# Kernel tuning notes

Measured on AMD Instinct MI355X. Metric: run time of the kernel, lower is better.

The kernel has to match this reference:

```python
import jax, jax.numpy as jnp
import numpy as np


def setup_inputs() -> dict:
    key = jax.random.key(0)
    k1, k2, k3, k4 = jax.random.split(key, 4)
    batch, T, state_dim, action_dim = 64, 1024, 512, 128
    x0 = jax.random.normal(k1, (batch, state_dim), dtype=jnp.float32)
    us = jax.random.normal(k2, (batch, T, action_dim), dtype=jnp.float32)
    # Scale A so the 1024-step linear recurrence stays bounded (spectral radius < 1)
    A = jax.random.normal(k3, (state_dim, state_dim), dtype=jnp.float32) * (0.9 / np.sqrt(state_dim))
    B = jax.random.normal(k4, (action_dim, state_dim), dtype=jnp.float32) * (1.0 / np.sqrt(action_dim))
    return {"x0": x0, "us": us, "A": A, "B": B}


def reference(x0, us, A, B):
    """Linear SSM rollout: x_{t+1} = x_t @ A + u_t @ B, returns xs [batch, T, state_dim]."""
    us_t = jnp.swapaxes(us, 0, 1)  # [T, batch, action_dim]

    def step(x, u):
        x_next = x @ A + u @ B  # [batch, state_dim]
        return x_next, x_next

    _, xs = jax.lax.scan(step, x0, us_t)  # xs: [T, batch, state_dim]
    return jnp.swapaxes(xs, 0, 1)  # [batch, T, state_dim]
```

## Files before the change

### kernel.cpp

```cpp
#include <hip/hip_runtime.h>


typedef __attribute__((ext_vector_type(8))) short bf16x8;
typedef __attribute__((ext_vector_type(8))) unsigned short ushort8;
typedef __attribute__((ext_vector_type(4))) float f32x4;
typedef unsigned short ushort_t;

#define MFMA16(a, b, c) __builtin_amdgcn_mfma_f32_16x16x32_bf16(a, b, c, 0, 0, 0)

#define OFF_AT  0UL
#define OFF_AU  8912896UL
#define OFF_BT  15204352UL
#define OFF_BU  15335424UL
#define OFF_WT  15466496UL
#define OFF_Z   16515072UL
#define OFF_E1S 41680896UL
#define OFF_E2S 50069504UL

__host__ __device__ __forceinline__ int slot_of(int p) {
    if (p == 0) return 16;
    if (p <= 8) return p - 1;
    return 7 + (p >> 3);
}

__device__ __forceinline__ unsigned short f2bf(float f) {
    union { float f; unsigned u; } v; v.f = f;
    unsigned r = v.u + 0x7FFFu + ((v.u >> 16) & 1u);
    return (unsigned short)(r >> 16);
}

__device__ __forceinline__ int sel4(int4 v, int p) {
    return p == 0 ? v.x : p == 1 ? v.y : p == 2 ? v.z : v.w;
}

typedef __attribute__((address_space(3))) unsigned int as3_u32;
typedef __attribute__((address_space(1))) const unsigned int as1_u32;
__device__ __forceinline__ void gll16(const void* g, void* l) {
    __builtin_amdgcn_global_load_lds((as1_u32*)g, (as3_u32*)l, 16, 0, 0);
}

__global__ __launch_bounds__(256) void prep_kernel(const float* __restrict__ x0,
                                                   const float* __restrict__ us,
                                                   const float* __restrict__ A,
                                                   const float* __restrict__ B,
                                                   char* __restrict__ ws) {
    ushort_t* At1 = (ushort_t*)(ws + OFF_AT);
    ushort_t* Au1 = (ushort_t*)(ws + OFF_AU);
    ushort_t* Bt  = (ushort_t*)(ws + OFF_BT);
    ushort_t* Bu  = (ushort_t*)(ws + OFF_BU);
    ushort_t* X0b = (ushort_t*)(ws + OFF_E2S);
    ushort_t* Z   = (ushort_t*)(ws + OFF_Z);
    long idx = (long)blockIdx.x * 256 + threadIdx.x;
    if (idx < 262144) {
        Au1[idx] = f2bf(A[idx]);
    } else if (idx < 524288) {
        long gi = idx - 262144;
        int n = (int)(gi >> 9), k = (int)(gi & 511);
        At1[gi] = f2bf(A[(long)k * 512 + n]);
    } else if (idx < 589824) {
        long i2 = idx - 524288;
        int kp = (int)(i2 >> 9), n = (int)(i2 & 511);
        ushort_t v = f2bf(B[i2]);
        Bt[(long)n * 128 + kp] = v;
        Bu[i2] = v;
    } else if (idx < 593920) {
        long gi = idx - 589824;
        long e0 = gi * 8;
        float4 v0 = *(const float4*)(x0 + e0);
        float4 v1 = *(const float4*)(x0 + e0 + 4);
        ushort8 h = { f2bf(v0.x), f2bf(v0.y), f2bf(v0.z), f2bf(v0.w),
                      f2bf(v1.x), f2bf(v1.y), f2bf(v1.z), f2bf(v1.w) };
        *(ushort8*)(X0b + e0) = h;
    } else if (idx < 1642496) {
        long gi = idx - 593920;
        int row = (int)(gi >> 7), g8 = (int)(gi & 127);
        int c = row >> 6, b = row & 63;
        const float* src = us + (long)b * 131072 + c * 1024 + g8 * 8;
        float4 v0 = *(const float4*)src;
        float4 v1 = *(const float4*)(src + 4);
        ushort8 h = { f2bf(v0.x), f2bf(v0.y), f2bf(v0.z), f2bf(v0.w),
                      f2bf(v1.x), f2bf(v1.y), f2bf(v1.z), f2bf(v1.w) };
        *(ushort8*)(Z + (long)row * 1536 + 512 + g8 * 8) = h;
    } else {
        long gi2 = idx - 1642496;
        if (gi2 < 262144) {
            int n = (int)(gi2 >> 9), k2 = (int)(gi2 & 511);
            At1[(long)16 * 262144 + gi2] = (n == k2) ? (ushort_t)0x3F80 : (ushort_t)0;
        }
    }
}

__device__ __forceinline__ void pow_tile(char* __restrict__ ws, ushort_t* ldsX,
                                         int d, int m_, int i_, int prod,
                                         int mb, int nb) {
    ushort_t* At = (ushort_t*)(ws + OFF_AT);
    ushort_t* Au = (ushort_t*)(ws + OFF_AU);
    const ushort_t *Xp, *Yp; ushort_t* outp;
    if (prod == 0) { Xp = At + (long)slot_of(m_) * 262144; Yp = Au + (long)slot_of(i_) * 262144; outp = At + (long)slot_of(d) * 262144; }
    else           { Xp = Au + (long)slot_of(i_) * 262144; Yp = At + (long)slot_of(m_) * 262144; outp = Au + (long)slot_of(d) * 262144; }

    int tid = threadIdx.x, w = tid >> 6, lane = tid & 63, q = lane >> 4, r = lane & 15;

    for (int i2 = tid; i2 < 64 * 64; i2 += 256) {
        int row = i2 >> 6, c8 = i2 & 63;
        ushort8 v = *(const ushort8*)(Xp + (long)(mb * 64 + row) * 512 + c8 * 8);
        *(ushort8*)&ldsX[row * 512 + ((c8 ^ (row & 7)) << 3)] = v;
    }
    __syncthreads();

    f32x4 acc[4][2];
    for (int a1 = 0; a1 < 4; a1++) for (int b1 = 0; b1 < 2; b1++) acc[a1][b1] = (f32x4){0.f, 0.f, 0.f, 0.f};

    int n0 = nb * 128 + w * 32;
    for (int kt = 0; kt < 16; kt++) {
        bf16x8 b0 = *(const bf16x8*)(Yp + (long)(n0 + r) * 512 + kt * 32 + q * 8);
        bf16x8 b1 = *(const bf16x8*)(Yp + (long)(n0 + 16 + r) * 512 + kt * 32 + q * 8);
        int g2 = kt * 4 + q;
#pragma unroll
        for (int mi = 0; mi < 4; mi++) {
            int row = mi * 16 + r;
            bf16x8 a = *(bf16x8*)&ldsX[row * 512 + ((g2 ^ (row & 7)) << 3)];
            acc[mi][0] = MFMA16(a, b0, acc[mi][0]);
            acc[mi][1] = MFMA16(a, b1, acc[mi][1]);
        }
    }
    for (int mi = 0; mi < 4; mi++) for (int nj = 0; nj < 2; nj++) {
        int m = mb * 64 + mi * 16 + q * 4, n = n0 + nj * 16 + r;
        for (int v = 0; v < 4; v++) outp[(long)(m + v) * 512 + n] = f2bf(acc[mi][nj][v]);
    }
}

__device__ __forceinline__ void wk_tile(char* __restrict__ ws, ushort_t* ldsX,
                                        int k8, int mb) {
    ushort_t* At = (ushort_t*)(ws + OFF_AT);
    ushort_t* Bu = (ushort_t*)(ws + OFF_BU);
    ushort_t* Bt = (ushort_t*)(ws + OFF_BT);
    ushort_t* Wt = (ushort_t*)(ws + OFF_WT);

    int tid = threadIdx.x, w = tid >> 6, lane = tid & 63, q = lane >> 4, r = lane & 15;

    if (k8 == 7) {
        for (int i2 = tid; i2 < 64 * 32; i2 += 256) {
            int row = i2 >> 5, c4 = i2 & 31;
            ushort4 v = *(const ushort4*)(Bt + (long)(mb * 64 + row) * 128 + c4 * 4);
            *(ushort4*)(Wt + (long)(mb * 64 + row) * 128 + c4 * 4) = v;
        }
        return;
    }

    int p = 7 - k8;
    const ushort_t* Xp = At + (long)slot_of(p) * 262144;
    for (int i2 = tid; i2 < 64 * 64; i2 += 256) {
        int row = i2 >> 6, c8 = i2 & 63;
        ushort8 v = *(const ushort8*)(Xp + (long)(mb * 64 + row) * 512 + c8 * 8);
        *(ushort8*)&ldsX[row * 512 + ((c8 ^ (row & 7)) << 3)] = v;
    }
    __syncthreads();

    f32x4 acc[4][2];
    for (int a1 = 0; a1 < 4; a1++) for (int b1 = 0; b1 < 2; b1++) acc[a1][b1] = (f32x4){0.f, 0.f, 0.f, 0.f};

    int n0 = w * 32;
    for (int kt = 0; kt < 16; kt++) {
        bf16x8 b0 = *(const bf16x8*)(Bu + (long)(n0 + r) * 512 + kt * 32 + q * 8);
        bf16x8 b1 = *(const bf16x8*)(Bu + (long)(n0 + 16 + r) * 512 + kt * 32 + q * 8);
        int g2 = kt * 4 + q;
#pragma unroll
        for (int mi = 0; mi < 4; mi++) {
            int row = mi * 16 + r;
            bf16x8 a = *(bf16x8*)&ldsX[row * 512 + ((g2 ^ (row & 7)) << 3)];
            acc[mi][0] = MFMA16(a, b0, acc[mi][0]);
            acc[mi][1] = MFMA16(a, b1, acc[mi][1]);
        }
    }
    ushort_t* Wp = Wt + (long)p * 65536;
    for (int mi = 0; mi < 4; mi++) for (int nj = 0; nj < 2; nj++) {
        int m = mb * 64 + mi * 16 + q * 4, n = n0 + nj * 16 + r;
        for (int v = 0; v < 4; v++) Wp[(long)(m + v) * 128 + n] = f2bf(acc[mi][nj][v]);
    }
}

__global__ __launch_bounds__(256) void pow_stage(char* __restrict__ ws,
                                                 int4 dd, int4 mm, int4 ii,
                                                 int dual, int wkbase) {
    __shared__ ushort_t ldsX[64 * 512];
    int bx = blockIdx.x;

    if (wkbase > 0 && bx >= wkbase) {
        int widx = bx - wkbase;
        wk_tile(ws, ldsX, widx >> 3, widx & 7);
        return;
    }

    int nb = bx & 3, mb = (bx >> 2) & 7;
    int prod, pair;
    if (dual) { prod = (bx >> 5) & 1; pair = bx >> 6; }
    else      { prod = 0;             pair = bx >> 5; }
    int d = sel4(dd, pair), m_ = sel4(mm, pair), i_ = sel4(ii, pair);
    pow_tile(ws, ldsX, d, m_, i_, prod, mb, nb);
}

__global__ __launch_bounds__(256, 4) void e1g(char* __restrict__ ws) {
    __shared__ ushort_t Alds[64 * 64];
    __shared__ ushort_t Blds[128 * 64];
    const ushort_t* Z  = (const ushort_t*)(ws + OFF_Z);
    const ushort_t* Wt = (const ushort_t*)(ws + OFF_WT);
    ushort_t* E1s = (ushort_t*)(ws + OFF_E1S);

    int bx = blockIdx.x;
    int c = bx >> 2, nt = bx & 3;
    int tid = threadIdx.x, w = tid >> 6, lane = tid & 63, q = lane >> 4, r = lane & 15;
    int wr = w >> 1, wc = w & 1;
    int l8 = lane >> 3, srcg = (lane & 7) ^ l8;

    const ushort_t* Xb = Z + (long)c * 64 * 1536 + 512;

    f32x4 acc[2][4];
#pragma unroll
    for (int a1 = 0; a1 < 2; a1++)
#pragma unroll
        for (int b1 = 0; b1 < 4; b1++) acc[a1][b1] = (f32x4){0.f, 0.f, 0.f, 0.f};

    for (int s = 0; s < 16; s++) {
        int k0 = s * 64;
#pragma unroll
        for (int i = 0; i < 2; i++) {
            int row = i * 32 + w * 8 + l8;
            gll16(Xb + (long)row * 1536 + k0 + srcg * 8, &Alds[i * 2048 + w * 512]);
        }
        const ushort_t* Yb = Wt + (long)(7 - (s >> 1)) * 65536 + (s & 1) * 64;
#pragma unroll
        for (int i = 0; i < 4; i++) {
            int row = i * 32 + w * 8 + l8;
            gll16(Yb + (long)(nt * 128 + row) * 128 + srcg * 8, &Blds[i * 2048 + w * 512]);
        }
        __syncthreads();
#pragma unroll
        for (int kt = 0; kt < 2; kt++) {
            int g2 = kt * 4 + q;
            bf16x8 a[2], b[4];
#pragma unroll
            for (int mi = 0; mi < 2; mi++) {
                int row = wr * 32 + mi * 16 + r;
                a[mi] = *(bf16x8*)&Alds[row * 64 + ((g2 ^ (row & 7)) << 3)];
            }
#pragma unroll
            for (int nj = 0; nj < 4; nj++) {
                int row = wc * 64 + nj * 16 + r;
                b[nj] = *(bf16x8*)&Blds[row * 64 + ((g2 ^ (row & 7)) << 3)];
            }
#pragma unroll
            for (int mi = 0; mi < 2; mi++)
#pragma unroll
                for (int nj = 0; nj < 4; nj++)
                    acc[mi][nj] = MFMA16(a[mi], b[nj], acc[mi][nj]);
        }
        __syncthreads();
    }

#pragma unroll
    for (int mi = 0; mi < 2; mi++)
#pragma unroll
        for (int nj = 0; nj < 4; nj++) {
            int m = wr * 32 + mi * 16 + q * 4;
            int n = nt * 128 + wc * 64 + nj * 16 + r;
#pragma unroll
            for (int v = 0; v < 4; v++)
                E1s[(long)c * 32768 + (long)(m + v) * 512 + n] = f2bf(acc[mi][nj][v]);
        }
}

__global__ __launch_bounds__(256, 4) void e2g(char* __restrict__ ws) {
    __shared__ ushort_t Alds[64 * 64];
    __shared__ ushort_t Blds[64 * 64];
    const ushort_t* At  = (const ushort_t*)(ws + OFF_AT);
    const ushort_t* E1s = (const ushort_t*)(ws + OFF_E1S);
    ushort_t* E2s = (ushort_t*)(ws + OFF_E2S);

    int bx = blockIdx.x;
    int g = bx >> 3, ntb = bx & 7;
    int tid = threadIdx.x, w = tid >> 6, lane = tid & 63, q = lane >> 4, r = lane & 15;
    int wr = w >> 1, wc = w & 1;
    int l8 = lane >> 3, srcg = (lane & 7) ^ l8;

    f32x4 acc[2][2];
#pragma unroll
    for (int a1 = 0; a1 < 2; a1++)
#pragma unroll
        for (int b1 = 0; b1 < 2; b1++) acc[a1][b1] = (f32x4){0.f, 0.f, 0.f, 0.f};

    for (int s = 0; s < 64; s++) {
        int t = s >> 3, k0 = (s & 7) * 64;
        const ushort_t* Xp = E1s + (long)(8 * g + t) * 32768;
        const ushort_t* Yb = At + (long)slot_of(8 * (7 - t)) * 262144;
#pragma unroll
        for (int i = 0; i < 2; i++) {
            int row = i * 32 + w * 8 + l8;
            gll16(Xp + (long)row * 512 + k0 + srcg * 8, &Alds[i * 2048 + w * 512]);
            gll16(Yb + (long)(ntb * 64 + row) * 512 + k0 + srcg * 8, &Blds[i * 2048 + w * 512]);
        }
        __syncthreads();
#pragma unroll
        for (int kt = 0; kt < 2; kt++) {
            int g2 = kt * 4 + q;
            bf16x8 a[2], b[2];
#pragma unroll
            for (int mi = 0; mi < 2; mi++) {
                int row = wr * 32 + mi * 16 + r;
                a[mi] = *(bf16x8*)&Alds[row * 64 + ((g2 ^ (row & 7)) << 3)];
            }
#pragma unroll
            for (int nj = 0; nj < 2; nj++) {
                int row = wc * 32 + nj * 16 + r;
                b[nj] = *(bf16x8*)&Blds[row * 64 + ((g2 ^ (row & 7)) << 3)];
            }
#pragma unroll
            for (int mi = 0; mi < 2; mi++)
#pragma unroll
                for (int nj = 0; nj < 2; nj++)
                    acc[mi][nj] = MFMA16(a[mi], b[nj], acc[mi][nj]);
        }
        __syncthreads();
    }

#pragma unroll
    for (int mi = 0; mi < 2; mi++)
#pragma unroll
        for (int nj = 0; nj < 2; nj++) {
            int m = wr * 32 + mi * 16 + q * 4;
            int n = ntb * 64 + wc * 32 + nj * 16 + r;
#pragma unroll
            for (int v = 0; v < 4; v++)
                E2s[(long)(1 + g) * 32768 + (long)(m + v) * 512 + n] = f2bf(acc[mi][nj][v]);
        }
}

__global__ __launch_bounds__(256, 4) void s1x(float* __restrict__ dout,
                                              char* __restrict__ ws) {
    __shared__ ushort_t Alds[64 * 64];
    __shared__ ushort_t Blds[128 * 64];
    const ushort_t* At  = (const ushort_t*)(ws + OFF_AT);
    const ushort_t* E1s = (const ushort_t*)(ws + OFF_E1S);
    const ushort_t* E2s = (const ushort_t*)(ws + OFF_E2S);
    ushort_t* Z = (ushort_t*)(ws + OFF_Z);

    int bx = blockIdx.x;
    int t0 = bx >> 2, nt = bx & 3;
    int g, j;
    if (t0 == 128) { g = 16; j = 0; }
    else {
        g = t0 >> 3;
        int jj = t0 & 7;
        j = (g >= 8) ? (7 - jj) : jj;
    }
    int c = g * 8 + j;
    int extra = (j == 0 && g >= 1) ? 1 : 0;
    int nterms = 1 + extra + j;
    int S = nterms * 8;
    int tid = threadIdx.x, w = tid >> 6, lane = tid & 63, q = lane >> 4, r = lane & 15;
    int wr = w >> 1, wc = w & 1;
    int l8 = lane >> 3, srcg = (lane & 7) ^ l8;

    auto xptr = [&](int t) -> const ushort_t* {
        if (t == 0) return E2s + (long)g * 32768;
        if (extra && t == 1) return E2s + (long)(g - 1) * 32768;
        return E1s + (long)(8 * g + t - 1 - extra) * 32768;
    };
    auto yptr = [&](int t) -> const ushort_t* {
        int p = (t == 0) ? 8 * j : ((extra && t == 1) ? 64 : 8 * (j - t + extra));
        return At + (long)slot_of(p) * 262144;
    };

    f32x4 acc[2][4];
#pragma unroll
    for (int a1 = 0; a1 < 2; a1++)
#pragma unroll
        for (int b1 = 0; b1 < 4; b1++) acc[a1][b1] = (f32x4){0.f, 0.f, 0.f, 0.f};

    for (int s = 0; s < S; s++) {
        int t = s >> 3, k0 = (s & 7) * 64;
        const ushort_t* Xp = xptr(t);
        const ushort_t* Yb = yptr(t);
#pragma unroll
        for (int i = 0; i < 2; i++) {
            int row = i * 32 + w * 8 + l8;
            gll16(Xp + (long)row * 512 + k0 + srcg * 8, &Alds[i * 2048 + w * 512]);
        }
#pragma unroll
        for (int i = 0; i < 4; i++) {
            int row = i * 32 + w * 8 + l8;
            gll16(Yb + (long)(nt * 128 + row) * 512 + k0 + srcg * 8, &Blds[i * 2048 + w * 512]);
        }
        __syncthreads();
#pragma unroll
        for (int kt = 0; kt < 2; kt++) {
            int g2 = kt * 4 + q;
            bf16x8 a[2], b[4];
#pragma unroll
            for (int mi = 0; mi < 2; mi++) {
                int row = wr * 32 + mi * 16 + r;
                a[mi] = *(bf16x8*)&Alds[row * 64 + ((g2 ^ (row & 7)) << 3)];
            }
#pragma unroll
            for (int nj = 0; nj < 4; nj++) {
                int row = wc * 64 + nj * 16 + r;
                b[nj] = *(bf16x8*)&Blds[row * 64 + ((g2 ^ (row & 7)) << 3)];
            }
#pragma unroll
            for (int mi = 0; mi < 2; mi++)
#pragma unroll
                for (int nj = 0; nj < 4; nj++)
                    acc[mi][nj] = MFMA16(a[mi], b[nj], acc[mi][nj]);
        }
        __syncthreads();
    }

#pragma unroll
    for (int mi = 0; mi < 2; mi++)
#pragma unroll
        for (int nj = 0; nj < 4; nj++) {
            int m = wr * 32 + mi * 16 + q * 4;
            int n = nt * 128 + wc * 64 + nj * 16 + r;
#pragma unroll
            for (int v = 0; v < 4; v++) {
                float val = acc[mi][nj][v];
                int row = m + v;
                if (c < 128)
                    Z[(long)(c * 64 + row) * 1536 + n] = f2bf(val);
                if (c >= 1)
                    dout[(long)row * 524288 + (long)(8 * c - 1) * 512 + n] = val;
            }
        }
}

__global__ __launch_bounds__(256, 4) void outg(float* __restrict__ dout,
                                               char* __restrict__ ws) {
    __shared__ ushort_t Alds[128 * 64];
    __shared__ ushort_t Blds[128 * 64];
    const ushort_t* Z  = (const ushort_t*)(ws + OFF_Z);
    const ushort_t* At = (const ushort_t*)(ws + OFF_AT);
    const ushort_t* Wt = (const ushort_t*)(ws + OFF_WT);

    int bx = blockIdx.x;
    int nt = bx / 448;
    int rem = bx - nt * 448;
    int k = rem >> 6;
    int mt = rem & 63;
    int tid = threadIdx.x, w = tid >> 6, lane = tid & 63, q = lane >> 4, r = lane & 15;
    int wr = w >> 1, wc = w & 1;
    int l8 = lane >> 3, srcg = (lane & 7) ^ l8;

    const ushort_t* Xb = Z + (long)mt * 128 * 1536;
    const ushort_t* Ya = At + (long)slot_of(k + 1) * 262144;
    int Ks = 8 + 2 * (k + 1);

    f32x4 acc[4][4];
#pragma unroll
    for (int a1 = 0; a1 < 4; a1++)
#pragma unroll
        for (int b1 = 0; b1 < 4; b1++) acc[a1][b1] = (f32x4){0.f, 0.f, 0.f, 0.f};

    for (int s = 0; s < Ks; s++) {
        int k0 = s * 64;
#pragma unroll
        for (int i = 0; i < 4; i++) {
            int row = i * 32 + w * 8 + l8;
            gll16(Xb + (long)row * 1536 + k0 + srcg * 8, &Alds[i * 2048 + w * 512]);
        }
        if (k0 < 512) {
#pragma unroll
            for (int i = 0; i < 4; i++) {
                int row = i * 32 + w * 8 + l8;
                gll16(Ya + (long)(nt * 128 + row) * 512 + k0 + srcg * 8, &Blds[i * 2048 + w * 512]);
            }
        } else {
            int uc = k0 - 512;
            const ushort_t* Yb = Wt + (long)(k - (uc >> 7)) * 65536 + (uc & 127);
#pragma unroll
            for (int i = 0; i < 4; i++) {
                int row = i * 32 + w * 8 + l8;
                gll16(Yb + (long)(nt * 128 + row) * 128 + srcg * 8, &Blds[i * 2048 + w * 512]);
            }
        }
        __syncthreads();
#pragma unroll
        for (int kt = 0; kt < 2; kt++) {
            int g2 = kt * 4 + q;
            bf16x8 a[4], b[4];
#pragma unroll
            for (int mi = 0; mi < 4; mi++) {
                int row = wr * 64 + mi * 16 + r;
                a[mi] = *(bf16x8*)&Alds[row * 64 + ((g2 ^ (row & 7)) << 3)];
            }
#pragma unroll
            for (int nj = 0; nj < 4; nj++) {
                int row = wc * 64 + nj * 16 + r;
                b[nj] = *(bf16x8*)&Blds[row * 64 + ((g2 ^ (row & 7)) << 3)];
            }
#pragma unroll
            for (int mi = 0; mi < 4; mi++)
#pragma unroll
                for (int nj = 0; nj < 4; nj++)
                    acc[mi][nj] = MFMA16(a[mi], b[nj], acc[mi][nj]);
        }
        __syncthreads();
    }

#pragma unroll
    for (int mi = 0; mi < 4; mi++) {
        int m = mt * 128 + wr * 64 + mi * 16 + q * 4;
#pragma unroll
        for (int nj = 0; nj < 4; nj++) {
            int n = nt * 128 + wc * 64 + nj * 16 + r;
#pragma unroll
            for (int v = 0; v < 4; v++) {
                int mm = m + v;
                dout[(long)(mm & 63) * 524288 + (long)(((mm >> 6) << 3) + k) * 512 + n] = acc[mi][nj][v];
            }
        }
    }
}

extern "C" void kernel_launch(void* const* d_in, const int* in_sizes, int n_in,
                              void* d_out, int out_size, void* d_ws, size_t ws_size,
                              hipStream_t stream) {
    const float* x0 = (const float*)d_in[0];
    const float* us = (const float*)d_in[1];
    const float* A  = (const float*)d_in[2];
    const float* B  = (const float*)d_in[3];
    float* dout = (float*)d_out;
    char* ws = (char*)d_ws;

    prep_kernel<<<7440, 256, 0, stream>>>(x0, us, A, B, ws);

    const int stn[6]     = {1, 2, 4, 1, 2, 4};
    const int stdual[6]  = {1, 1, 1, 1, 1, 0};
    const int stwk[6]    = {0, 0, 0, 64, 0, 0};
    const int std_[6][4] = {{2,0,0,0},{3,4,0,0},{5,6,7,8},{16,0,0,0},{24,32,0,0},{40,48,56,64}};
    const int stm[6][4]  = {{1,0,0,0},{2,2,0,0},{4,4,4,4},{8,0,0,0},{16,16,0,0},{32,32,32,32}};
    const int sti[6][4]  = {{1,0,0,0},{1,2,0,0},{1,2,3,4},{8,0,0,0},{8,16,0,0},{8,16,24,32}};
    for (int s = 0; s < 6; s++) {
        int4 dd = {std_[s][0], std_[s][1], std_[s][2], std_[s][3]};
        int4 mm = {stm[s][0], stm[s][1], stm[s][2], stm[s][3]};
        int4 ii = {sti[s][0], sti[s][1], sti[s][2], sti[s][3]};
        int blocks = stn[s] * (stdual[s] ? 64 : 32) + (stwk[s] ? 64 : 0);
        pow_stage<<<blocks, 256, 0, stream>>>(ws, dd, mm, ii, stdual[s], stwk[s]);
    }

    e1g<<<512, 256, 0, stream>>>(ws);
    e2g<<<128, 256, 0, stream>>>(ws);
    s1x<<<516, 256, 0, stream>>>(dout, ws);
    outg<<<1792, 256, 0, stream>>>(dout, ws);
}
```

Before: 258.7 us.

## Fold E1 GEMM into later power-stage launches to fill idle CUs

```diff
diff --git a/kernel.cpp b/kernel.cpp
--- a/kernel.cpp
+++ b/kernel.cpp
@@ -180,12 +180,88 @@
     }
 }
 
+__device__ __forceinline__ void e1_tile(char* __restrict__ ws, ushort_t* lds,
+                                        int mt, int nt) {
+    ushort_t* Alds = lds;
+    ushort_t* Blds = lds + 8192;
+    const ushort_t* Z  = (const ushort_t*)(ws + OFF_Z);
+    const ushort_t* Wt = (const ushort_t*)(ws + OFF_WT);
+    ushort_t* E1s = (ushort_t*)(ws + OFF_E1S);
+
+    int tid = threadIdx.x, w = tid >> 6, lane = tid & 63, q = lane >> 4, r = lane & 15;
+    int wr = w >> 1, wc = w & 1;
+    int l8 = lane >> 3, srcg = (lane & 7) ^ l8;
+
+    const ushort_t* Xb = Z + (long)mt * 128 * 1536 + 512;
+
+    f32x4 acc[4][4];
+#pragma unroll
+    for (int a1 = 0; a1 < 4; a1++)
+#pragma unroll
+        for (int b1 = 0; b1 < 4; b1++) acc[a1][b1] = (f32x4){0.f, 0.f, 0.f, 0.f};
+
+    for (int s = 0; s < 16; s++) {
+        int k0 = s * 64;
+#pragma unroll
+        for (int i = 0; i < 4; i++) {
+            int row = i * 32 + w * 8 + l8;
+            gll16(Xb + (long)row * 1536 + k0 + srcg * 8, &Alds[i * 2048 + w * 512]);
+        }
+        const ushort_t* Yb = Wt + (long)(7 - (s >> 1)) * 65536 + (s & 1) * 64;
+#pragma unroll
+        for (int i = 0; i < 4; i++) {
+            int row = i * 32 + w * 8 + l8;
+            gll16(Yb + (long)(nt * 128 + row) * 128 + srcg * 8, &Blds[i * 2048 + w * 512]);
+        }
+        __syncthreads();
+#pragma unroll
+        for (int kt = 0; kt < 2; kt++) {
+            int g2 = kt * 4 + q;
+            bf16x8 a[4], b[4];
+#pragma unroll
+            for (int mi = 0; mi < 4; mi++) {
+                int row = wr * 64 + mi * 16 + r;
+                a[mi] = *(bf16x8*)&Alds[row * 64 + ((g2 ^ (row & 7)) << 3)];
+            }
+#pragma unroll
+            for (int nj = 0; nj < 4; nj++) {
+                int row = wc * 64 + nj * 16 + r;
+                b[nj] = *(bf16x8*)&Blds[row * 64 + ((g2 ^ (row & 7)) << 3)];
+            }
+#pragma unroll
+            for (int mi = 0; mi < 4; mi++)
+#pragma unroll
+                for (int nj = 0; nj < 4; nj++)
+                    acc[mi][nj] = MFMA16(a[mi], b[nj], acc[mi][nj]);
+        }
+        __syncthreads();
+    }
+
+#pragma unroll
+    for (int mi = 0; mi < 4; mi++) {
+        int m = mt * 128 + wr * 64 + mi * 16 + q * 4;
+#pragma unroll
+        for (int nj = 0; nj < 4; nj++) {
+            int n = nt * 128 + wc * 64 + nj * 16 + r;
+#pragma unroll
+            for (int v = 0; v < 4; v++)
+                E1s[(long)(m + v) * 512 + n] = f2bf(acc[mi][nj][v]);
+        }
+    }
+}
+
 __global__ __launch_bounds__(256) void pow_stage(char* __restrict__ ws,
                                                  int4 dd, int4 mm, int4 ii,
-                                                 int dual, int wkbase) {
+                                                 int dual, int wkbase,
+                                                 int e1base, int e1mtoff) {
     __shared__ ushort_t ldsX[64 * 512];
     int bx = blockIdx.x;
 
+    if (e1base > 0 && bx >= e1base) {
+        int idx = bx - e1base;
+        e1_tile(ws, ldsX, e1mtoff + (idx >> 2), idx & 3);
+        return;
+    }
     if (wkbase > 0 && bx >= wkbase) {
         int widx = bx - wkbase;
         wk_tile(ws, ldsX, widx >> 3, widx & 7);
@@ -198,76 +274,6 @@
     else      { prod = 0;             pair = bx >> 5; }
     int d = sel4(dd, pair), m_ = sel4(mm, pair), i_ = sel4(ii, pair);
     pow_tile(ws, ldsX, d, m_, i_, prod, mb, nb);
-}
-
-__global__ __launch_bounds__(256, 4) void e1g(char* __restrict__ ws) {
-    __shared__ ushort_t Alds[64 * 64];
-    __shared__ ushort_t Blds[128 * 64];
-    const ushort_t* Z  = (const ushort_t*)(ws + OFF_Z);
-    const ushort_t* Wt = (const ushort_t*)(ws + OFF_WT);
-    ushort_t* E1s = (ushort_t*)(ws + OFF_E1S);
-
-    int bx = blockIdx.x;
-    int c = bx >> 2, nt = bx & 3;
-    int tid = threadIdx.x, w = tid >> 6, lane = tid & 63, q = lane >> 4, r = lane & 15;
-    int wr = w >> 1, wc = w & 1;
-    int l8 = lane >> 3, srcg = (lane & 7) ^ l8;
-
-    const ushort_t* Xb = Z + (long)c * 64 * 1536 + 512;
-
-    f32x4 acc[2][4];
-#pragma unroll
-    for (int a1 = 0; a1 < 2; a1++)
-#pragma unroll
-        for (int b1 = 0; b1 < 4; b1++) acc[a1][b1] = (f32x4){0.f, 0.f, 0.f, 0.f};
-
-    for (int s = 0; s < 16; s++) {
-        int k0 = s * 64;
-#pragma unroll
-        for (int i = 0; i < 2; i++) {
-            int row = i * 32 + w * 8 + l8;
-            gll16(Xb + (long)row * 1536 + k0 + srcg * 8, &Alds[i * 2048 + w * 512]);
-        }
-        const ushort_t* Yb = Wt + (long)(7 - (s >> 1)) * 65536 + (s & 1) * 64;
-#pragma unroll
-        for (int i = 0; i < 4; i++) {
-            int row = i * 32 + w * 8 + l8;
-            gll16(Yb + (long)(nt * 128 + row) * 128 + srcg * 8, &Blds[i * 2048 + w * 512]);
-        }
-        __syncthreads();
-#pragma unroll
-        for (int kt = 0; kt < 2; kt++) {
-            int g2 = kt * 4 + q;
-            bf16x8 a[2], b[4];
-#pragma unroll
-            for (int mi = 0; mi < 2; mi++) {
-                int row = wr * 32 + mi * 16 + r;
-                a[mi] = *(bf16x8*)&Alds[row * 64 + ((g2 ^ (row & 7)) << 3)];
-            }
-#pragma unroll
-            for (int nj = 0; nj < 4; nj++) {
-                int row = wc * 64 + nj * 16 + r;
-                b[nj] = *(bf16x8*)&Blds[row * 64 + ((g2 ^ (row & 7)) << 3)];
-            }
-#pragma unroll
-            for (int mi = 0; mi < 2; mi++)
-#pragma unroll
-                for (int nj = 0; nj < 4; nj++)
-                    acc[mi][nj] = MFMA16(a[mi], b[nj], acc[mi][nj]);
-        }
-        __syncthreads();
-    }
-
-#pragma unroll
-    for (int mi = 0; mi < 2; mi++)
-#pragma unroll
-        for (int nj = 0; nj < 4; nj++) {
-            int m = wr * 32 + mi * 16 + q * 4;
-            int n = nt * 128 + wc * 64 + nj * 16 + r;
-#pragma unroll
-            for (int v = 0; v < 4; v++)
-                E1s[(long)c * 32768 + (long)(m + v) * 512 + n] = f2bf(acc[mi][nj][v]);
-        }
 }
 
 __global__ __launch_bounds__(256, 4) void e2g(char* __restrict__ ws) {
@@ -536,6 +542,8 @@
     const int stn[6]     = {1, 2, 4, 1, 2, 4};
     const int stdual[6]  = {1, 1, 1, 1, 1, 0};
     const int stwk[6]    = {0, 0, 0, 64, 0, 0};
+    const int ste1[6]    = {0, 0, 0, 0, 128, 128};
+    const int ste1m[6]   = {0, 0, 0, 0, 0, 32};
     const int std_[6][4] = {{2,0,0,0},{3,4,0,0},{5,6,7,8},{16,0,0,0},{24,32,0,0},{40,48,56,64}};
     const int stm[6][4]  = {{1,0,0,0},{2,2,0,0},{4,4,4,4},{8,0,0,0},{16,16,0,0},{32,32,32,32}};
     const int sti[6][4]  = {{1,0,0,0},{1,2,0,0},{1,2,3,4},{8,0,0,0},{8,16,0,0},{8,16,24,32}};
@@ -543,11 +551,11 @@
         int4 dd = {std_[s][0], std_[s][1], std_[s][2], std_[s][3]};
         int4 mm = {stm[s][0], stm[s][1], stm[s][2], stm[s][3]};
         int4 ii = {sti[s][0], sti[s][1], sti[s][2], sti[s][3]};
-        int blocks = stn[s] * (stdual[s] ? 64 : 32) + (stwk[s] ? 64 : 0);
-        pow_stage<<<blocks, 256, 0, stream>>>(ws, dd, mm, ii, stdual[s], stwk[s]);
-    }
-
-    e1g<<<512, 256, 0, stream>>>(ws);
+        int blocks = stn[s] * (stdual[s] ? 64 : 32) + (stwk[s] ? 64 : 0) + (ste1[s] ? 128 : 0);
+        pow_stage<<<blocks, 256, 0, stream>>>(ws, dd, mm, ii, stdual[s], stwk[s],
+                                              ste1[s], ste1m[s]);
+    }
+
     e2g<<<128, 256, 0, stream>>>(ws);
     s1x<<<516, 256, 0, stream>>>(dout, ws);
     outg<<<1792, 256, 0, stream>>>(dout, ws);
```

Result: no change. 263.7 us (+1.9%).

## Overlap us bf16 conversion with power stages and split e2g tiles finer

Applied to the files above, without the earlier changes.

```diff
diff --git a/kernel.cpp b/kernel.cpp
--- a/kernel.cpp
+++ b/kernel.cpp
@@ -40,7 +40,6 @@
 }
 
 __global__ __launch_bounds__(256) void prep_kernel(const float* __restrict__ x0,
-                                                   const float* __restrict__ us,
                                                    const float* __restrict__ A,
                                                    const float* __restrict__ B,
                                                    char* __restrict__ ws) {
@@ -49,7 +48,6 @@
     ushort_t* Bt  = (ushort_t*)(ws + OFF_BT);
     ushort_t* Bu  = (ushort_t*)(ws + OFF_BU);
     ushort_t* X0b = (ushort_t*)(ws + OFF_E2S);
-    ushort_t* Z   = (ushort_t*)(ws + OFF_Z);
     long idx = (long)blockIdx.x * 256 + threadIdx.x;
     if (idx < 262144) {
         Au1[idx] = f2bf(A[idx]);
@@ -71,18 +69,8 @@
         ushort8 h = { f2bf(v0.x), f2bf(v0.y), f2bf(v0.z), f2bf(v0.w),
                       f2bf(v1.x), f2bf(v1.y), f2bf(v1.z), f2bf(v1.w) };
         *(ushort8*)(X0b + e0) = h;
-    } else if (idx < 1642496) {
-        long gi = idx - 593920;
-        int row = (int)(gi >> 7), g8 = (int)(gi & 127);
-        int c = row >> 6, b = row & 63;
-        const float* src = us + (long)b * 131072 + c * 1024 + g8 * 8;
-        float4 v0 = *(const float4*)src;
-        float4 v1 = *(const float4*)(src + 4);
-        ushort8 h = { f2bf(v0.x), f2bf(v0.y), f2bf(v0.z), f2bf(v0.w),
-                      f2bf(v1.x), f2bf(v1.y), f2bf(v1.z), f2bf(v1.w) };
-        *(ushort8*)(Z + (long)row * 1536 + 512 + g8 * 8) = h;
     } else {
-        long gi2 = idx - 1642496;
+        long gi2 = idx - 593920;
         if (gi2 < 262144) {
             int n = (int)(gi2 >> 9), k2 = (int)(gi2 & 511);
             At1[(long)16 * 262144 + gi2] = (n == k2) ? (ushort_t)0x3F80 : (ushort_t)0;
@@ -181,11 +169,29 @@
 }
 
 __global__ __launch_bounds__(256) void pow_stage(char* __restrict__ ws,
+                                                 const float* __restrict__ us,
                                                  int4 dd, int4 mm, int4 ii,
-                                                 int dual, int wkbase) {
+                                                 int dual, int wkbase,
+                                                 int ubase, int ustart, int uend) {
     __shared__ ushort_t ldsX[64 * 512];
     int bx = blockIdx.x;
 
+    if (ubase > 0 && bx >= ubase) {
+        ushort_t* Z = (ushort_t*)(ws + OFF_Z);
+        int tid = threadIdx.x;
+        int nthr = (256 - ubase) * 256;
+        for (long gi = ustart + (long)(bx - ubase) * 256 + tid; gi < uend; gi += nthr) {
+            int row = (int)(gi >> 7), g8 = (int)(gi & 127);
+            int c = row >> 6, b = row & 63;
+            const float* src = us + (long)b * 131072 + c * 1024 + g8 * 8;
+            float4 v0 = *(const float4*)src;
+            float4 v1 = *(const float4*)(src + 4);
+            ushort8 h = { f2bf(v0.x), f2bf(v0.y), f2bf(v0.z), f2bf(v0.w),
+                          f2bf(v1.x), f2bf(v1.y), f2bf(v1.z), f2bf(v1.w) };
+            *(ushort8*)(Z + (long)row * 1536 + 512 + g8 * 8) = h;
+        }
+        return;
+    }
     if (wkbase > 0 && bx >= wkbase) {
         int widx = bx - wkbase;
         wk_tile(ws, ldsX, widx >> 3, widx & 7);
@@ -272,22 +278,20 @@
 
 __global__ __launch_bounds__(256, 4) void e2g(char* __restrict__ ws) {
     __shared__ ushort_t Alds[64 * 64];
-    __shared__ ushort_t Blds[64 * 64];
+    __shared__ ushort_t Blds[32 * 64];
     const ushort_t* At  = (const ushort_t*)(ws + OFF_AT);
     const ushort_t* E1s = (const ushort_t*)(ws + OFF_E1S);
     ushort_t* E2s = (ushort_t*)(ws + OFF_E2S);
 
     int bx = blockIdx.x;
-    int g = bx >> 3, ntb = bx & 7;
+    int g = bx >> 4, ntb = bx & 15;
     int tid = threadIdx.x, w = tid >> 6, lane = tid & 63, q = lane >> 4, r = lane & 15;
     int wr = w >> 1, wc = w & 1;
     int l8 = lane >> 3, srcg = (lane & 7) ^ l8;
 
-    f32x4 acc[2][2];
-#pragma unroll
-    for (int a1 = 0; a1 < 2; a1++)
-#pragma unroll
-        for (int b1 = 0; b1 < 2; b1++) acc[a1][b1] = (f32x4){0.f, 0.f, 0.f, 0.f};
+    f32x4 acc[2][1];
+#pragma unroll
+    for (int a1 = 0; a1 < 2; a1++) acc[a1][0] = (f32x4){0.f, 0.f, 0.f, 0.f};
 
     for (int s = 0; s < 64; s++) {
         int t = s >> 3, k0 = (s & 7) * 64;
@@ -297,42 +301,40 @@
         for (int i = 0; i < 2; i++) {
             int row = i * 32 + w * 8 + l8;
             gll16(Xp + (long)row * 512 + k0 + srcg * 8, &Alds[i * 2048 + w * 512]);
-            gll16(Yb + (long)(ntb * 64 + row) * 512 + k0 + srcg * 8, &Blds[i * 2048 + w * 512]);
+        }
+        {
+            int row = w * 8 + l8;
+            gll16(Yb + (long)(ntb * 32 + row) * 512 + k0 + srcg * 8, &Blds[w * 512]);
         }
         __syncthreads();
 #pragma unroll
         for (int kt = 0; kt < 2; kt++) {
             int g2 = kt * 4 + q;
-            bf16x8 a[2], b[2];
+            bf16x8 a[2], b;
 #pragma unroll
             for (int mi = 0; mi < 2; mi++) {
                 int row = wr * 32 + mi * 16 + r;
                 a[mi] = *(bf16x8*)&Alds[row * 64 + ((g2 ^ (row & 7)) << 3)];
             }
-#pragma unroll
-            for (int nj = 0; nj < 2; nj++) {
-                int row = wc * 32 + nj * 16 + r;
-                b[nj] = *(bf16x8*)&Blds[row * 64 + ((g2 ^ (row & 7)) << 3)];
+            {
+                int row = wc * 16 + r;
+                b = *(bf16x8*)&Blds[row * 64 + ((g2 ^ (row & 7)) << 3)];
             }
 #pragma unroll
             for (int mi = 0; mi < 2; mi++)
-#pragma unroll
-                for (int nj = 0; nj < 2; nj++)
-                    acc[mi][nj] = MFMA16(a[mi], b[nj], acc[mi][nj]);
-        }
-        __syncthreads();
-    }
-
-#pragma unroll
-    for (int mi = 0; mi < 2; mi++)
-#pragma unroll
-        for (int nj = 0; nj < 2; nj++) {
-            int m = wr * 32 + mi * 16 + q * 4;
-            int n = ntb * 64 + wc * 32 + nj * 16 + r;
-#pragma unroll
-            for (int v = 0; v < 4; v++)
-                E2s[(long)(1 + g) * 32768 + (long)(m + v) * 512 + n] = f2bf(acc[mi][nj][v]);
-        }
+                acc[mi][0] = MFMA16(a[mi], b, acc[mi][0]);
+        }
+        __syncthreads();
+    }
+
+#pragma unroll
+    for (int mi = 0; mi < 2; mi++) {
+        int m = wr * 32 + mi * 16 + q * 4;
+        int n = ntb * 32 + wc * 16 + r;
+#pragma unroll
+        for (int v = 0; v < 4; v++)
+            E2s[(long)(1 + g) * 32768 + (long)(m + v) * 512 + n] = f2bf(acc[mi][0][v]);
+    }
 }
 
 __global__ __launch_bounds__(256, 4) void s1x(float* __restrict__ dout,
@@ -531,11 +533,14 @@
     float* dout = (float*)d_out;
     char* ws = (char*)d_ws;
 
-    prep_kernel<<<7440, 256, 0, stream>>>(x0, us, A, B, ws);
-
-    const int stn[6]     = {1, 2, 4, 1, 2, 4};
+    prep_kernel<<<3344, 256, 0, stream>>>(x0, A, B, ws);
+
+    const int stpw[6]    = {64, 128, 256, 64, 128, 128};
     const int stdual[6]  = {1, 1, 1, 1, 1, 0};
     const int stwk[6]    = {0, 0, 0, 64, 0, 0};
+    const int stub[6]    = {64, 128, 0, 128, 128, 128};
+    const int stus[6]    = {0, 262144, 0, 458752, 655360, 851968};
+    const int stue[6]    = {262144, 458752, 0, 655360, 851968, 1048576};
     const int std_[6][4] = {{2,0,0,0},{3,4,0,0},{5,6,7,8},{16,0,0,0},{24,32,0,0},{40,48,56,64}};
     const int stm[6][4]  = {{1,0,0,0},{2,2,0,0},{4,4,4,4},{8,0,0,0},{16,16,0,0},{32,32,32,32}};
     const int sti[6][4]  = {{1,0,0,0},{1,2,0,0},{1,2,3,4},{8,0,0,0},{8,16,0,0},{8,16,24,32}};
@@ -543,12 +548,13 @@
         int4 dd = {std_[s][0], std_[s][1], std_[s][2], std_[s][3]};
         int4 mm = {stm[s][0], stm[s][1], stm[s][2], stm[s][3]};
         int4 ii = {sti[s][0], sti[s][1], sti[s][2], sti[s][3]};
-        int blocks = stn[s] * (stdual[s] ? 64 : 32) + (stwk[s] ? 64 : 0);
-        pow_stage<<<blocks, 256, 0, stream>>>(ws, dd, mm, ii, stdual[s], stwk[s]);
+        int blocks = (stub[s] > 0) ? 256 : stpw[s] + stwk[s];
+        pow_stage<<<blocks, 256, 0, stream>>>(ws, us, dd, mm, ii, stdual[s],
+                                              stwk[s], stub[s], stus[s], stue[s]);
     }
 
     e1g<<<512, 256, 0, stream>>>(ws);
-    e2g<<<128, 256, 0, stream>>>(ws);
+    e2g<<<256, 256, 0, stream>>>(ws);
     s1x<<<516, 256, 0, stream>>>(dout, ws);
     outg<<<1792, 256, 0, stream>>>(dout, ws);
 }
```

Measured after the change: 253.0 us. 2.2% less time.
